# Performance work log

Hardware: AMD Instinct MI355X
Metric: run time of the kernel (lower is better)

The kernel has to match this reference:

```python
import jax, jax.numpy as jnp
import numpy as np

N_NODES = 50000
N_EDGES = 1000000
F = 256          # feature_size
NC = 300         # n_content_dims
ED = 64          # embedding_dim = 2**int(log2(F/4))
L = 3            # n_layers


def setup_inputs() -> dict:
    key = jax.random.key(0)
    ks = jax.random.split(key, 20)
    s = 0.05  # weight init scale
    return {
        'node_ids': jnp.arange(N_NODES, dtype=jnp.int32),
        'content': jax.random.normal(ks[0], (N_NODES, NC), jnp.float32),
        'src': jax.random.randint(ks[1], (N_EDGES,), 0, N_NODES, jnp.int32),
        'dst': jax.random.randint(ks[2], (N_EDGES,), 0, N_NODES, jnp.int32),
        'emb': jax.random.normal(ks[3], (N_NODES + 1, ED), jnp.float32) / ED,
        'W_exp': jax.random.normal(ks[4], (F, ED), jnp.float32) * s,
        'b_exp': jnp.zeros((F,), jnp.float32),
        'W_p1': jax.random.normal(ks[5], (NC, NC), jnp.float32) * s,
        'b_p1': jnp.zeros((NC,), jnp.float32),
        'W_p2': jax.random.normal(ks[6], (F, NC), jnp.float32) * s,
        'b_p2': jnp.zeros((F,), jnp.float32),
        'W_conv': jax.random.normal(ks[7], (L, F, 2 * F), jnp.float32) * s,
        'b_conv': jnp.zeros((L, F), jnp.float32),
        'Wo1': jax.random.normal(ks[8], (L - 1, F, F), jnp.float32) * s,
        'bo1': jnp.zeros((L - 1, F), jnp.float32),
        'Wo2': jax.random.normal(ks[9], (L - 1, F, F), jnp.float32) * s,
        'bo2': jnp.zeros((L - 1, F), jnp.float32),
    }


def _lrelu(x):
    return jax.nn.leaky_relu(x, 0.1)


def reference(node_ids, content, src, dst, emb, W_exp, b_exp, W_p1, b_p1,
              W_p2, b_p2, W_conv, b_conv, Wo1, bo1, Wo2, bo2):
    # initial node repr: expansion(node_emb) + proj(content)  (GaussianNoise = identity at eval)
    h = _lrelu(emb[node_ids] @ W_exp.T + b_exp)                 # [N, F]
    c = _lrelu(content @ W_p1.T + b_p1)
    c = _lrelu(c @ W_p2.T + b_p2)
    h = h + c

    ones = jnp.ones((src.shape[0],), h.dtype)
    deg = jax.ops.segment_sum(ones, dst, num_segments=N_NODES)  # in-degree
    w = (deg + 1.0)[:, None]                                    # +1 for self-loop

    for i in range(L):
        # message passing: sum neighbor h (with self-loop), then neighbor mean
        agg = jax.ops.segment_sum(h[src], dst, num_segments=N_NODES) + h  # [N, F]
        h_agg = (agg - h) / jnp.maximum(w - 1.0, 1.0)
        h_concat = jnp.concatenate([h, h_agg], axis=1)          # [N, 2F]
        h_new = h_concat @ W_conv[i].T + b_conv[i]
        if i < L - 1:
            h_new = _lrelu(h_new)
        # L2-normalize rows
        h_new = h_new / jnp.maximum(
            jnp.linalg.norm(h_new, axis=1, keepdims=True), 1e-6)
        if i < L - 1:  # W_out block (non-prediction layers)
            h_new = _lrelu(h_new @ Wo1[i].T + bo1[i])
            h_new = h_new @ Wo2[i].T + bo2[i]
        h = h_new
    return h
```

## Files before the change

kernel.cpp:

```cpp
#include <hip/hip_runtime.h>
#include <stdint.h>

#define NNODES 50000
#define NROWS_PAD 50048
#define NEDGES 1000000
#define FD 256
#define NCPAD 384
#define EDIM 64
#define NSCAN ((NNODES + 255) / 256)

typedef unsigned short u16;
typedef __attribute__((ext_vector_type(8))) short short8;
typedef __attribute__((ext_vector_type(4))) float floatx4;

__device__ __forceinline__ float bf2f(u16 x) {
    union { unsigned u; float f; } c; c.u = ((unsigned)x) << 16; return c.f;
}
__device__ __forceinline__ u16 f2bf(float f) {
    union { float f; unsigned u; } c; c.f = f;
    unsigned u = c.u;
    return (u16)((u + 0x7fffu + ((u >> 16) & 1u)) >> 16);
}
__device__ __forceinline__ void gload16(const u16* g, u16* l) {
    __builtin_amdgcn_global_load_lds(
        (const __attribute__((address_space(1))) void*)g,
        (__attribute__((address_space(3))) void*)l, 16, 0, 0);
}

__global__ void detect_kernel(const u16* p, int* flag) {
    __shared__ int smax;
    if (threadIdx.x == 0) smax = 0;
    __syncthreads();
    int m = 0;
    for (int i = threadIdx.x; i < 8192; i += 256) {
        int e = (p[i] >> 7) & 0xFF;
        m = m > e ? m : e;
    }
    atomicMax(&smax, m);
    __syncthreads();
    if (threadIdx.x == 0) *flag = (smax >= 140) ? 1 : 0;
}

#define NB_CONV 1798
#define NB_PADC 37536
#define NB_PADE 6256
#define NB_CNT  1954
#define NB_OTH  (NB_CONV + NB_PADC + NB_PADE)
#define PREP_GRID 47572
__global__ __launch_bounds__(512) void prep_kernel(
    u16* arena, const int* flagp,
    const void* wexp, const void* bexp, const void* wp1, const void* bp1,
    const void* wp2, const void* bp2, const void* wconv, const void* bconv,
    const void* wo1, const void* bo1, const void* wo2, const void* bo2,
    u16* cpad, const void* content, u16* ebuf, const void* emb,
    const int* dst, int* deg)
{
    const int bid = blockIdx.x;
    const int q = bid / 24, r = bid % 24;
    if (r == 23) {
        if (q >= NB_CNT) return;
        int e = q * 512 + threadIdx.x;
        if (e < NEDGES) atomicAdd(&deg[dst[e]], 1);
        return;
    }
    long oid = (long)q * 23 + r;
    if (oid >= NB_OTH) return;
    int fl = *flagp;
    if (oid < NB_CONV) {
        const int offs[13]  = {0,16384,16640,164096,164480,262784,263040,
                               656256,657024,788096,788608,919680,920192};
        const int rreal[12] = {256,1,300,1,256,1,768,1,512,1,512,1};
        const int creal[12] = {64,256,300,300,300,256,512,768,256,512,256,512};
        const int cpd[12]   = {64,256,384,384,384,256,512,768,256,512,256,512};
        long gid = oid * 512 + threadIdx.x;
        if (gid >= 920192) return;
        const void* srcs[12] = {wexp,bexp,wp1,bp1,wp2,bp2,wconv,bconv,wo1,bo1,wo2,bo2};
        int t = 0;
        #pragma unroll
        for (int i = 1; i < 12; ++i) if (gid >= offs[i]) t = i;
        long local = gid - offs[t];
        int rr = (int)(local / cpd[t]);
        int cc = (int)(local % cpd[t]);
        u16 v = 0;
        if (rr < rreal[t] && cc < creal[t]) {
            long si = (long)rr * creal[t] + cc;
            v = fl ? f2bf(((const float*)srcs[t])[si]) : ((const u16*)srcs[t])[si];
        }
        arena[gid] = v;
    } else if (oid < NB_CONV + NB_PADC) {
        long gid = (oid - NB_CONV) * 512 + threadIdx.x;
        int rr = (int)(gid / NCPAD), cc = (int)(gid % NCPAD);
        u16 v = 0;
        if (rr < NNODES && cc < 300) {
            long si = (long)rr * 300 + cc;
            v = fl ? f2bf(((const float*)content)[si]) : ((const u16*)content)[si];
        }
        cpad[gid] = v;
    } else {
        long gid = (oid - NB_CONV - NB_PADC) * 512 + threadIdx.x;
        int rr = (int)(gid / EDIM), cc = (int)(gid % EDIM);
        u16 v = 0;
        if (rr < NNODES) {
            long si = (long)rr * EDIM + cc;
            v = fl ? f2bf(((const float*)emb)[si]) : ((const u16*)emb)[si];
        }
        ebuf[gid] = v;
    }
}

__global__ __launch_bounds__(256) void scan1_kernel(const int* deg, int* bsum) {
    __shared__ int s[256];
    int t = threadIdx.x;
    int i = blockIdx.x * 256 + t;
    s[t] = (i < NNODES) ? deg[i] : 0;
    __syncthreads();
    #pragma unroll
    for (int off = 128; off > 0; off >>= 1) {
        if (t < off) s[t] += s[t + off];
        __syncthreads();
    }
    if (t == 0) bsum[blockIdx.x] = s[0];
}

__global__ __launch_bounds__(256) void scan2_kernel(int* bsum, int* row_start) {
    __shared__ int s[256];
    int t = threadIdx.x;
    int v = (t < NSCAN) ? bsum[t] : 0;
    s[t] = v;
    __syncthreads();
    for (int off = 1; off < 256; off <<= 1) {
        int x = (t >= off) ? s[t - off] : 0;
        __syncthreads();
        s[t] += x;
        __syncthreads();
    }
    if (t < NSCAN) bsum[t] = s[t] - v;
    if (t == 0) row_start[NNODES] = NEDGES;
}

__global__ __launch_bounds__(256) void scan3_kernel(const int* deg, const int* bsum,
        int* row_start, int* cursor, float* inv_w) {
    __shared__ int s[256];
    int t = threadIdx.x;
    int i = blockIdx.x * 256 + t;
    int v = (i < NNODES) ? deg[i] : 0;
    s[t] = v;
    __syncthreads();
    for (int off = 1; off < 256; off <<= 1) {
        int x = (t >= off) ? s[t - off] : 0;
        __syncthreads();
        s[t] += x;
        __syncthreads();
    }
    if (i < NNODES) {
        int base = bsum[blockIdx.x] + s[t] - v;
        row_start[i] = base;
        cursor[i] = base;
        inv_w[i] = 1.0f / (float)(v > 0 ? v : 1);
    }
}

#define IF_GRID (391 * 7)
__global__ __launch_bounds__(512, 4) void initfill_kernel(
    const u16* __restrict__ cpad, const u16* __restrict__ ebuf,
    const u16* __restrict__ Wp1, const u16* __restrict__ bp1,
    const u16* __restrict__ Wp2, const u16* __restrict__ bp2,
    const u16* __restrict__ Wexp, const u16* __restrict__ bexp,
    u16* __restrict__ hbuf,
    const int* __restrict__ src, const int* __restrict__ dst,
    int* __restrict__ cursor, int* __restrict__ esrc)
{
    __shared__ __align__(16) u16 sA[64 * 32];
    __shared__ __align__(16) u16 sB[384 * 32];
    __shared__ __align__(16) u16 T[64 * 384];

    const int g7 = blockIdx.x / 7, r7 = blockIdx.x % 7;
    if (r7 >= 2) {
        int fb = g7 * 5 + (r7 - 2);
        int e = fb * 512 + threadIdx.x;
        if (e < NEDGES) {
            int v = dst[e];
            int pos = atomicAdd(&cursor[v], 1);
            if ((unsigned)pos < (unsigned)NEDGES) esrc[pos] = src[e];
        }
        return;
    }
    const int bm = (g7 * 2 + r7) * 64;
    const int t = threadIdx.x;
    const int wave = t >> 6, lane = t & 63;
    const int quad = lane >> 4, l16 = lane & 15;
    const int wm = wave >> 2, wn = wave & 3;
    const int lrow = lane >> 2, lcol = (lane & 3) * 8;

    floatx4 a1[2][6];
    #pragma unroll
    for (int i = 0; i < 2; ++i)
        #pragma unroll
        for (int j = 0; j < 6; ++j) a1[i][j] = (floatx4){0.f, 0.f, 0.f, 0.f};
    for (int kt = 0; kt < 384; kt += 32) {
        if (wave < 4)
            gload16(cpad + (size_t)(bm + wave * 16 + lrow) * NCPAD + kt + lcol,
                    &sA[(wave * 16) * 32]);
        #pragma unroll
        for (int c = 0; c < 3; ++c) {
            int r0 = wave * 48 + c * 16;
            gload16(Wp1 + (size_t)(r0 + lrow) * NCPAD + kt + lcol, &sB[r0 * 32]);
        }
        __syncthreads();
        short8 af[2];
        #pragma unroll
        for (int mt = 0; mt < 2; ++mt)
            af[mt] = *(const short8*)&sA[(wm * 32 + mt * 16 + l16) * 32 + quad * 8];
        #pragma unroll
        for (int nt = 0; nt < 6; ++nt) {
            short8 bf = *(const short8*)&sB[(wn * 96 + nt * 16 + l16) * 32 + quad * 8];
            a1[0][nt] = __builtin_amdgcn_mfma_f32_16x16x32_bf16(af[0], bf, a1[0][nt], 0, 0, 0);
            a1[1][nt] = __builtin_amdgcn_mfma_f32_16x16x32_bf16(af[1], bf, a1[1][nt], 0, 0, 0);
        }
        __syncthreads();
    }
    #pragma unroll
    for (int nt = 0; nt < 6; ++nt) {
        int col = wn * 96 + nt * 16 + l16;
        float bv = bf2f(bp1[col]);
        #pragma unroll
        for (int mt = 0; mt < 2; ++mt)
            #pragma unroll
            for (int rr = 0; rr < 4; ++rr) {
                int row = wm * 32 + mt * 16 + quad * 4 + rr;
                float v = a1[mt][nt][rr] + bv;
                v = v > 0.f ? v : 0.1f * v;
                T[(row * NCPAD + col) ^ ((row & 7) << 3)] = f2bf(v);
            }
    }
    __syncthreads();

    floatx4 a2[2][4];
    #pragma unroll
    for (int i = 0; i < 2; ++i)
        #pragma unroll
        for (int j = 0; j < 4; ++j) a2[i][j] = (floatx4){0.f, 0.f, 0.f, 0.f};
    for (int kt = 0; kt < 384; kt += 32) {
        #pragma unroll
        for (int c = 0; c < 2; ++c) {
            int r0 = wave * 32 + c * 16;
            gload16(Wp2 + (size_t)(r0 + lrow) * NCPAD + kt + lcol, &sB[r0 * 32]);
        }
        __syncthreads();
        short8 af[2];
        #pragma unroll
        for (int mt = 0; mt < 2; ++mt) {
            int row = wm * 32 + mt * 16 + l16;
            af[mt] = *(const short8*)&T[(row * NCPAD + kt + quad * 8) ^ ((row & 7) << 3)];
        }
        #pragma unroll
        for (int nt = 0; nt < 4; ++nt) {
            short8 bf = *(const short8*)&sB[(wn * 64 + nt * 16 + l16) * 32 + quad * 8];
            a2[0][nt] = __builtin_amdgcn_mfma_f32_16x16x32_bf16(af[0], bf, a2[0][nt], 0, 0, 0);
            a2[1][nt] = __builtin_amdgcn_mfma_f32_16x16x32_bf16(af[1], bf, a2[1][nt], 0, 0, 0);
        }
        __syncthreads();
    }

    floatx4 aE[2][4];
    #pragma unroll
    for (int i = 0; i < 2; ++i)
        #pragma unroll
        for (int j = 0; j < 4; ++j) aE[i][j] = (floatx4){0.f, 0.f, 0.f, 0.f};
    for (int kt = 0; kt < 64; kt += 32) {
        if (wave < 4)
            gload16(ebuf + (size_t)(bm + wave * 16 + lrow) * EDIM + kt + lcol,
                    &sA[(wave * 16) * 32]);
        #pragma unroll
        for (int c = 0; c < 2; ++c) {
            int r0 = wave * 32 + c * 16;
            gload16(Wexp + (size_t)(r0 + lrow) * EDIM + kt + lcol, &sB[r0 * 32]);
        }
        __syncthreads();
        short8 af[2];
        #pragma unroll
        for (int mt = 0; mt < 2; ++mt)
            af[mt] = *(const short8*)&sA[(wm * 32 + mt * 16 + l16) * 32 + quad * 8];
        #pragma unroll
        for (int nt = 0; nt < 4; ++nt) {
            short8 bf = *(const short8*)&sB[(wn * 64 + nt * 16 + l16) * 32 + quad * 8];
            aE[0][nt] = __builtin_amdgcn_mfma_f32_16x16x32_bf16(af[0], bf, aE[0][nt], 0, 0, 0);
            aE[1][nt] = __builtin_amdgcn_mfma_f32_16x16x32_bf16(af[1], bf, aE[1][nt], 0, 0, 0);
        }
        __syncthreads();
    }

    #pragma unroll
    for (int nt = 0; nt < 4; ++nt) {
        int col = wn * 64 + nt * 16 + l16;
        float bE = bf2f(bexp[col]), b2 = bf2f(bp2[col]);
        #pragma unroll
        for (int mt = 0; mt < 2; ++mt)
            #pragma unroll
            for (int rr = 0; rr < 4; ++rr) {
                int row = wm * 32 + mt * 16 + quad * 4 + rr;
                int gm = bm + row;
                if (gm < NNODES) {
                    float hE = aE[mt][nt][rr] + bE; hE = hE > 0.f ? hE : 0.1f * hE;
                    float c2 = a2[mt][nt][rr] + b2; c2 = c2 > 0.f ? c2 : 0.1f * c2;
                    hbuf[(size_t)gm * FD + col] = f2bf(hE + c2);
                }
            }
    }
}

__global__ __launch_bounds__(512, 4) void layer_kernel(
    const u16* __restrict__ h, const u16* __restrict__ agg,
    const u16* __restrict__ Wc, const u16* __restrict__ bc,
    const u16* __restrict__ W1, const u16* __restrict__ b1,
    const u16* __restrict__ W2, const u16* __restrict__ b2,
    u16* __restrict__ out)
{
    __shared__ __align__(16) u16 sA[2][64 * 32];
    __shared__ __align__(16) u16 sB[2][256 * 32];
    __shared__ __align__(16) u16 T[64 * 256];
    __shared__ float ssq[4][64];

    const int t = threadIdx.x;
    const int wave = t >> 6, lane = t & 63;
    const int quad = lane >> 4, l16 = lane & 15;
    const int wm = wave >> 2, wn = wave & 3;
    const int lrow = lane >> 2, lcol = (lane & 3) * 8;
    const int bm = blockIdx.x * 64;

    floatx4 acc[2][4];
    #pragma unroll
    for (int i = 0; i < 2; ++i)
        #pragma unroll
        for (int j = 0; j < 4; ++j) acc[i][j] = (floatx4){0.f, 0.f, 0.f, 0.f};

    for (int kt = 0; kt < 512; kt += 64) {
        const u16* Ap = (kt < 256) ? h : agg;
        const int kk = kt & 255;
        {
            int hh = wave & 1, r0 = (wave >> 1) * 16;
            gload16(Ap + (size_t)(bm + r0 + lrow) * 256 + kk + hh * 32 + lcol,
                    &sA[hh][r0 * 32]);
        }
        #pragma unroll
        for (int c = 0; c < 4; ++c) {
            int hh = c >> 1, r0 = wave * 32 + (c & 1) * 16;
            gload16(Wc + (size_t)(r0 + lrow) * 512 + kt + hh * 32 + lcol,
                    &sB[hh][r0 * 32]);
        }
        __syncthreads();
        #pragma unroll
        for (int g = 0; g < 2; ++g) {
            short8 af[2], bf[4];
            #pragma unroll
            for (int mt = 0; mt < 2; ++mt)
                af[mt] = *(const short8*)&sA[g][(wm * 32 + mt * 16 + l16) * 32 + quad * 8];
            #pragma unroll
            for (int nt = 0; nt < 4; ++nt)
                bf[nt] = *(const short8*)&sB[g][(wn * 64 + nt * 16 + l16) * 32 + quad * 8];
            #pragma unroll
            for (int mt = 0; mt < 2; ++mt)
                #pragma unroll
                for (int nt = 0; nt < 4; ++nt)
                    acc[mt][nt] = __builtin_amdgcn_mfma_f32_16x16x32_bf16(af[mt], bf[nt], acc[mt][nt], 0, 0, 0);
        }
        __syncthreads();
    }
    {
        float part[2][4];
        #pragma unroll
        for (int mt = 0; mt < 2; ++mt)
            #pragma unroll
            for (int rr = 0; rr < 4; ++rr) part[mt][rr] = 0.f;
        #pragma unroll
        for (int nt = 0; nt < 4; ++nt) {
            float bv = bf2f(bc[wn * 64 + nt * 16 + l16]);
            #pragma unroll
            for (int mt = 0; mt < 2; ++mt)
                #pragma unroll
                for (int rr = 0; rr < 4; ++rr) {
                    float v = acc[mt][nt][rr] + bv;
                    v = v > 0.f ? v : 0.1f * v;
                    part[mt][rr] += v * v;
                }
        }
        #pragma unroll
        for (int off = 1; off < 16; off <<= 1)
            #pragma unroll
            for (int mt = 0; mt < 2; ++mt)
                #pragma unroll
                for (int rr = 0; rr < 4; ++rr)
                    part[mt][rr] += __shfl_xor(part[mt][rr], off);
        if (l16 == 0)
            #pragma unroll
            for (int mt = 0; mt < 2; ++mt)
                #pragma unroll
                for (int rr = 0; rr < 4; ++rr)
                    ssq[wn][wm * 32 + mt * 16 + quad * 4 + rr] = part[mt][rr];
        __syncthreads();
        #pragma unroll
        for (int mt = 0; mt < 2; ++mt)
            #pragma unroll
            for (int rr = 0; rr < 4; ++rr) {
                int row = wm * 32 + mt * 16 + quad * 4 + rr;
                float s = 1.0f / fmaxf(sqrtf(ssq[0][row] + ssq[1][row] +
                                             ssq[2][row] + ssq[3][row]), 1e-6f);
                #pragma unroll
                for (int nt = 0; nt < 4; ++nt) {
                    int col = wn * 64 + nt * 16 + l16;
                    float v = acc[mt][nt][rr] + bf2f(bc[col]);
                    v = v > 0.f ? v : 0.1f * v;
                    T[(row * 256 + col) ^ ((row & 7) << 3)] = f2bf(v * s);
                }
            }
        __syncthreads();
    }

    #pragma unroll
    for (int i = 0; i < 2; ++i)
        #pragma unroll
        for (int j = 0; j < 4; ++j) acc[i][j] = (floatx4){0.f, 0.f, 0.f, 0.f};
    for (int kt = 0; kt < 256; kt += 64) {
        #pragma unroll
        for (int c = 0; c < 4; ++c) {
            int hh = c >> 1, r0 = wave * 32 + (c & 1) * 16;
            gload16(W1 + (size_t)(r0 + lrow) * 256 + kt + hh * 32 + lcol,
                    &sB[hh][r0 * 32]);
        }
        __syncthreads();
        #pragma unroll
        for (int g = 0; g < 2; ++g) {
            short8 af[2], bf[4];
            #pragma unroll
            for (int mt = 0; mt < 2; ++mt) {
                int row = wm * 32 + mt * 16 + l16;
                af[mt] = *(const short8*)&T[(row * 256 + kt + g * 32 + quad * 8) ^ ((row & 7) << 3)];
            }
            #pragma unroll
            for (int nt = 0; nt < 4; ++nt)
                bf[nt] = *(const short8*)&sB[g][(wn * 64 + nt * 16 + l16) * 32 + quad * 8];
            #pragma unroll
            for (int mt = 0; mt < 2; ++mt)
                #pragma unroll
                for (int nt = 0; nt < 4; ++nt)
                    acc[mt][nt] = __builtin_amdgcn_mfma_f32_16x16x32_bf16(af[mt], bf[nt], acc[mt][nt], 0, 0, 0);
        }
        __syncthreads();
    }
    #pragma unroll
    for (int nt = 0; nt < 4; ++nt) {
        int col = wn * 64 + nt * 16 + l16;
        float bv = bf2f(b1[col]);
        #pragma unroll
        for (int mt = 0; mt < 2; ++mt) {
            #pragma unroll
            for (int r = 0; r < 4; ++r) {
                int row = wm * 32 + mt * 16 + quad * 4 + r;
                float v = acc[mt][nt][r] + bv;
                v = v > 0.f ? v : 0.1f * v;
                T[(row * 256 + col) ^ ((row & 7) << 3)] = f2bf(v);
            }
        }
    }
    __syncthreads();

    #pragma unroll
    for (int i = 0; i < 2; ++i)
        #pragma unroll
        for (int j = 0; j < 4; ++j) acc[i][j] = (floatx4){0.f, 0.f, 0.f, 0.f};
    for (int kt = 0; kt < 256; kt += 64) {
        #pragma unroll
        for (int c = 0; c < 4; ++c) {
            int hh = c >> 1, r0 = wave * 32 + (c & 1) * 16;
            gload16(W2 + (size_t)(r0 + lrow) * 256 + kt + hh * 32 + lcol,
                    &sB[hh][r0 * 32]);
        }
        __syncthreads();
        #pragma unroll
        for (int g = 0; g < 2; ++g) {
            short8 af[2], bf[4];
            #pragma unroll
            for (int mt = 0; mt < 2; ++mt) {
                int row = wm * 32 + mt * 16 + l16;
                af[mt] = *(const short8*)&T[(row * 256 + kt + g * 32 + quad * 8) ^ ((row & 7) << 3)];
            }
            #pragma unroll
            for (int nt = 0; nt < 4; ++nt)
                bf[nt] = *(const short8*)&sB[g][(wn * 64 + nt * 16 + l16) * 32 + quad * 8];
            #pragma unroll
            for (int mt = 0; mt < 2; ++mt)
                #pragma unroll
                for (int nt = 0; nt < 4; ++nt)
                    acc[mt][nt] = __builtin_amdgcn_mfma_f32_16x16x32_bf16(af[mt], bf[nt], acc[mt][nt], 0, 0, 0);
        }
        __syncthreads();
    }
    #pragma unroll
    for (int nt = 0; nt < 4; ++nt) {
        int col = wn * 64 + nt * 16 + l16;
        float bv = bf2f(b2[col]);
        #pragma unroll
        for (int mt = 0; mt < 2; ++mt) {
            #pragma unroll
            for (int r = 0; r < 4; ++r) {
                int row = wm * 32 + mt * 16 + quad * 4 + r;
                int gm = bm + row;
                if (gm < NNODES) {
                    float v = acc[mt][nt][r] + bv;
                    out[(size_t)gm * 256 + col] = f2bf(v);
                }
            }
        }
    }
}

__global__ __launch_bounds__(512, 4) void final_kernel(
    const u16* __restrict__ h, const u16* __restrict__ agg,
    const u16* __restrict__ Wc, const u16* __restrict__ bc,
    float* __restrict__ out)
{
    __shared__ __align__(16) u16 sA[2][64 * 32];
    __shared__ __align__(16) u16 sB[2][256 * 32];
    __shared__ float ssq[4][64];

    const int t = threadIdx.x;
    const int wave = t >> 6, lane = t & 63;
    const int quad = lane >> 4, l16 = lane & 15;
    const int wm = wave >> 2, wn = wave & 3;
    const int lrow = lane >> 2, lcol = (lane & 3) * 8;
    const int bm = blockIdx.x * 64;

    floatx4 acc[2][4];
    #pragma unroll
    for (int i = 0; i < 2; ++i)
        #pragma unroll
        for (int j = 0; j < 4; ++j) acc[i][j] = (floatx4){0.f, 0.f, 0.f, 0.f};

    for (int kt = 0; kt < 512; kt += 64) {
        const u16* Ap = (kt < 256) ? h : agg;
        const int kk = kt & 255;
        {
            int hh = wave & 1, r0 = (wave >> 1) * 16;
            gload16(Ap + (size_t)(bm + r0 + lrow) * 256 + kk + hh * 32 + lcol,
                    &sA[hh][r0 * 32]);
        }
        #pragma unroll
        for (int c = 0; c < 4; ++c) {
            int hh = c >> 1, r0 = wave * 32 + (c & 1) * 16;
            gload16(Wc + (size_t)(r0 + lrow) * 512 + kt + hh * 32 + lcol,
                    &sB[hh][r0 * 32]);
        }
        __syncthreads();
        #pragma unroll
        for (int g = 0; g < 2; ++g) {
            short8 af[2], bf[4];
            #pragma unroll
            for (int mt = 0; mt < 2; ++mt)
                af[mt] = *(const short8*)&sA[g][(wm * 32 + mt * 16 + l16) * 32 + quad * 8];
            #pragma unroll
            for (int nt = 0; nt < 4; ++nt)
                bf[nt] = *(const short8*)&sB[g][(wn * 64 + nt * 16 + l16) * 32 + quad * 8];
            #pragma unroll
            for (int mt = 0; mt < 2; ++mt)
                #pragma unroll
                for (int nt = 0; nt < 4; ++nt)
                    acc[mt][nt] = __builtin_amdgcn_mfma_f32_16x16x32_bf16(af[mt], bf[nt], acc[mt][nt], 0, 0, 0);
        }
        __syncthreads();
    }
    float part[2][4];
    #pragma unroll
    for (int mt = 0; mt < 2; ++mt)
        #pragma unroll
        for (int rr = 0; rr < 4; ++rr) part[mt][rr] = 0.f;
    #pragma unroll
    for (int nt = 0; nt < 4; ++nt) {
        float bv = bf2f(bc[wn * 64 + nt * 16 + l16]);
        #pragma unroll
        for (int mt = 0; mt < 2; ++mt)
            #pragma unroll
            for (int rr = 0; rr < 4; ++rr) {
                float v = acc[mt][nt][rr] + bv;
                part[mt][rr] += v * v;
            }
    }
    #pragma unroll
    for (int off = 1; off < 16; off <<= 1)
        #pragma unroll
        for (int mt = 0; mt < 2; ++mt)
            #pragma unroll
            for (int rr = 0; rr < 4; ++rr)
                part[mt][rr] += __shfl_xor(part[mt][rr], off);
    if (l16 == 0)
        #pragma unroll
        for (int mt = 0; mt < 2; ++mt)
            #pragma unroll
            for (int rr = 0; rr < 4; ++rr)
                ssq[wn][wm * 32 + mt * 16 + quad * 4 + rr] = part[mt][rr];
    __syncthreads();
    #pragma unroll
    for (int mt = 0; mt < 2; ++mt)
        #pragma unroll
        for (int rr = 0; rr < 4; ++rr) {
            int row = wm * 32 + mt * 16 + quad * 4 + rr;
            int gm = bm + row;
            float s = 1.0f / fmaxf(sqrtf(ssq[0][row] + ssq[1][row] +
                                         ssq[2][row] + ssq[3][row]), 1e-6f);
            if (gm < NNODES) {
                #pragma unroll
                for (int nt = 0; nt < 4; ++nt) {
                    int col = wn * 64 + nt * 16 + l16;
                    out[(size_t)gm * 256 + col] = (acc[mt][nt][rr] + bf2f(bc[col])) * s;
                }
            }
        }
}

__global__ __launch_bounds__(256) void agg_kernel(
    const u16* h, const int* row_start, const int* esrc,
    const float* inv_w, u16* out)
{
    int gid = blockIdx.x * blockDim.x + threadIdx.x;
    int wid = gid >> 6;
    int lane = gid & 63;
    if (wid >= NNODES) return;
    int e0 = row_start[wid], e1 = row_start[wid + 1];
    e0 = max(0, min(e0, NEDGES));
    e1 = max(e0, min(e1, NEDGES));
    float a0 = 0.f, a1 = 0.f, a2 = 0.f, a3 = 0.f;
    int e = e0;
    for (; e + 4 <= e1; e += 4) {
        int u0 = esrc[e + 0]; if ((unsigned)u0 >= (unsigned)NNODES) u0 = 0;
        int u1 = esrc[e + 1]; if ((unsigned)u1 >= (unsigned)NNODES) u1 = 0;
        int u2 = esrc[e + 2]; if ((unsigned)u2 >= (unsigned)NNODES) u2 = 0;
        int u3 = esrc[e + 3]; if ((unsigned)u3 >= (unsigned)NNODES) u3 = 0;
        ushort4 t0 = *(const ushort4*)(h + (size_t)u0 * FD + lane * 4);
        ushort4 t1 = *(const ushort4*)(h + (size_t)u1 * FD + lane * 4);
        ushort4 t2 = *(const ushort4*)(h + (size_t)u2 * FD + lane * 4);
        ushort4 t3 = *(const ushort4*)(h + (size_t)u3 * FD + lane * 4);
        a0 += bf2f(t0.x) + bf2f(t1.x) + bf2f(t2.x) + bf2f(t3.x);
        a1 += bf2f(t0.y) + bf2f(t1.y) + bf2f(t2.y) + bf2f(t3.y);
        a2 += bf2f(t0.z) + bf2f(t1.z) + bf2f(t2.z) + bf2f(t3.z);
        a3 += bf2f(t0.w) + bf2f(t1.w) + bf2f(t2.w) + bf2f(t3.w);
    }
    for (; e < e1; ++e) {
        int u = esrc[e];
        if ((unsigned)u >= (unsigned)NNODES) u = 0;
        ushort4 tv = *(const ushort4*)(h + (size_t)u * FD + lane * 4);
        a0 += bf2f(tv.x); a1 += bf2f(tv.y); a2 += bf2f(tv.z); a3 += bf2f(tv.w);
    }
    float s = inv_w[wid];
    ushort4 ov;
    ov.x = f2bf(a0 * s); ov.y = f2bf(a1 * s); ov.z = f2bf(a2 * s); ov.w = f2bf(a3 * s);
    *(ushort4*)(out + (size_t)wid * FD + lane * 4) = ov;
}

extern "C" void kernel_launch(void* const* d_in, const int* in_sizes, int n_in,
                              void* d_out, int out_size, void* d_ws, size_t ws_size,
                              hipStream_t stream) {
    const void* content = d_in[1];
    const int* src      = (const int*)d_in[2];
    const int* dst      = (const int*)d_in[3];
    const void* emb     = d_in[4];

    char* ws = (char*)d_ws;
    u16* arena = (u16*)(ws);
    u16* hbuf  = (u16*)(ws + 1840640);
    u16* buf2  = (u16*)(ws + 27465216);
    u16* cpad  = (u16*)(ws + 27465216);
    u16* ebuf  = (u16*)(ws + 65902336);
    int*   deg    = (int*)(ws + 78714368);
    int*   rs     = (int*)(ws + 78914560);
    int*   cursor = (int*)(ws + 79114752);
    float* inv_w  = (float*)(ws + 79314944);
    int*   esrc   = (int*)(ws + 79515136);
    int*   bsum   = (int*)(ws + 83515648);
    int*   flag   = (int*)(ws + 83516672);

    u16* aWexp  = arena;            u16* aBexp  = arena + 16384;
    u16* aWp1   = arena + 16640;    u16* aBp1   = arena + 164096;
    u16* aWp2   = arena + 164480;   u16* aBp2   = arena + 262784;
    u16* aWconv = arena + 263040;   u16* aBconv = arena + 656256;
    u16* aWo1   = arena + 657024;   u16* aBo1   = arena + 788096;
    u16* aWo2   = arena + 788608;   u16* aBo2   = arena + 919680;

    const int MB64 = NROWS_PAD / 64;

    detect_kernel<<<1, 256, 0, stream>>>((const u16*)content, flag);
    hipMemsetAsync(deg, 0, (size_t)NNODES * 4, stream);
    prep_kernel<<<PREP_GRID, 512, 0, stream>>>(arena, flag,
        d_in[5], d_in[6], d_in[7], d_in[8], d_in[9], d_in[10], d_in[11],
        d_in[12], d_in[13], d_in[14], d_in[15], d_in[16],
        cpad, content, ebuf, emb, dst, deg);

    scan1_kernel<<<NSCAN, 256, 0, stream>>>(deg, bsum);
    scan2_kernel<<<1, 256, 0, stream>>>(bsum, rs);
    scan3_kernel<<<NSCAN, 256, 0, stream>>>(deg, bsum, rs, cursor, inv_w);

    initfill_kernel<<<IF_GRID, 512, 0, stream>>>(cpad, ebuf,
        aWp1, aBp1, aWp2, aBp2, aWexp, aBexp, hbuf, src, dst, cursor, esrc);

    for (int i = 0; i < 3; ++i) {
        agg_kernel<<<(NNODES * 64) / 256, 256, 0, stream>>>(hbuf, rs, esrc, inv_w, buf2);
        if (i < 2) {
            layer_kernel<<<dim3(MB64), dim3(512), 0, stream>>>(
                hbuf, buf2,
                aWconv + (size_t)i * FD * 2 * FD, aBconv + (size_t)i * FD,
                aWo1 + (size_t)i * FD * FD, aBo1 + (size_t)i * FD,
                aWo2 + (size_t)i * FD * FD, aBo2 + (size_t)i * FD,
                hbuf);
        } else {
            final_kernel<<<dim3(MB64), dim3(512), 0, stream>>>(
                hbuf, buf2,
                aWconv + (size_t)i * FD * 2 * FD, aBconv + (size_t)i * FD,
                (float*)d_out);
        }
    }
}
```

Before: 688.3 us.

## Fuse content/embedding conversion into initfill and vectorize degree counting

```diff
diff --git a/kernel.cpp b/kernel.cpp
--- a/kernel.cpp
+++ b/kernel.cpp
@@ -42,70 +42,48 @@
 }
 
 #define NB_CONV 1798
-#define NB_PADC 37536
-#define NB_PADE 6256
-#define NB_CNT  1954
-#define NB_OTH  (NB_CONV + NB_PADC + NB_PADE)
-#define PREP_GRID 47572
+#define NB_CNT4 489
+#define PREP_GRID (NB_CONV + NB_CNT4)
 __global__ __launch_bounds__(512) void prep_kernel(
     u16* arena, const int* flagp,
     const void* wexp, const void* bexp, const void* wp1, const void* bp1,
     const void* wp2, const void* bp2, const void* wconv, const void* bconv,
     const void* wo1, const void* bo1, const void* wo2, const void* bo2,
-    u16* cpad, const void* content, u16* ebuf, const void* emb,
     const int* dst, int* deg)
 {
     const int bid = blockIdx.x;
-    const int q = bid / 24, r = bid % 24;
-    if (r == 23) {
-        if (q >= NB_CNT) return;
-        int e = q * 512 + threadIdx.x;
-        if (e < NEDGES) atomicAdd(&deg[dst[e]], 1);
+    if (bid >= NB_CONV) {
+        int q4 = (bid - NB_CONV) * 512 + threadIdx.x;
+        if (q4 * 4 + 3 < NEDGES) {
+            int4 d = *(const int4*)(dst + q4 * 4);
+            atomicAdd(&deg[d.x], 1);
+            atomicAdd(&deg[d.y], 1);
+            atomicAdd(&deg[d.z], 1);
+            atomicAdd(&deg[d.w], 1);
+        }
         return;
     }
-    long oid = (long)q * 23 + r;
-    if (oid >= NB_OTH) return;
+    const int offs[13]  = {0,16384,16640,164096,164480,262784,263040,
+                           656256,657024,788096,788608,919680,920192};
+    const int rreal[12] = {256,1,300,1,256,1,768,1,512,1,512,1};
+    const int creal[12] = {64,256,300,300,300,256,512,768,256,512,256,512};
+    const int cpd[12]   = {64,256,384,384,384,256,512,768,256,512,256,512};
+    long gid = (long)bid * 512 + threadIdx.x;
+    if (gid >= 920192) return;
+    const void* srcs[12] = {wexp,bexp,wp1,bp1,wp2,bp2,wconv,bconv,wo1,bo1,wo2,bo2};
     int fl = *flagp;
-    if (oid < NB_CONV) {
-        const int offs[13]  = {0,16384,16640,164096,164480,262784,263040,
-                               656256,657024,788096,788608,919680,920192};
-        const int rreal[12] = {256,1,300,1,256,1,768,1,512,1,512,1};
-        const int creal[12] = {64,256,300,300,300,256,512,768,256,512,256,512};
-        const int cpd[12]   = {64,256,384,384,384,256,512,768,256,512,256,512};
-        long gid = oid * 512 + threadIdx.x;
-        if (gid >= 920192) return;
-        const void* srcs[12] = {wexp,bexp,wp1,bp1,wp2,bp2,wconv,bconv,wo1,bo1,wo2,bo2};
-        int t = 0;
-        #pragma unroll
-        for (int i = 1; i < 12; ++i) if (gid >= offs[i]) t = i;
-        long local = gid - offs[t];
-        int rr = (int)(local / cpd[t]);
-        int cc = (int)(local % cpd[t]);
-        u16 v = 0;
-        if (rr < rreal[t] && cc < creal[t]) {
-            long si = (long)rr * creal[t] + cc;
-            v = fl ? f2bf(((const float*)srcs[t])[si]) : ((const u16*)srcs[t])[si];
-        }
-        arena[gid] = v;
-    } else if (oid < NB_CONV + NB_PADC) {
-        long gid = (oid - NB_CONV) * 512 + threadIdx.x;
-        int rr = (int)(gid / NCPAD), cc = (int)(gid % NCPAD);
-        u16 v = 0;
-        if (rr < NNODES && cc < 300) {
-            long si = (long)rr * 300 + cc;
-            v = fl ? f2bf(((const float*)content)[si]) : ((const u16*)content)[si];
-        }
-        cpad[gid] = v;
-    } else {
-        long gid = (oid - NB_CONV - NB_PADC) * 512 + threadIdx.x;
-        int rr = (int)(gid / EDIM), cc = (int)(gid % EDIM);
-        u16 v = 0;
-        if (rr < NNODES) {
-            long si = (long)rr * EDIM + cc;
-            v = fl ? f2bf(((const float*)emb)[si]) : ((const u16*)emb)[si];
-        }
-        ebuf[gid] = v;
-    }
+    int t = 0;
+    #pragma unroll
+    for (int i = 1; i < 12; ++i) if (gid >= offs[i]) t = i;
+    long local = gid - offs[t];
+    int rr = (int)(local / cpd[t]);
+    int cc = (int)(local % cpd[t]);
+    u16 v = 0;
+    if (rr < rreal[t] && cc < creal[t]) {
+        long si = (long)rr * creal[t] + cc;
+        v = fl ? f2bf(((const float*)srcs[t])[si]) : ((const u16*)srcs[t])[si];
+    }
+    arena[gid] = v;
 }
 
 __global__ __launch_bounds__(256) void scan1_kernel(const int* deg, int* bsum) {
@@ -162,7 +140,8 @@
 
 #define IF_GRID (391 * 7)
 __global__ __launch_bounds__(512, 4) void initfill_kernel(
-    const u16* __restrict__ cpad, const u16* __restrict__ ebuf,
+    const void* __restrict__ content, const void* __restrict__ emb,
+    const int* __restrict__ flagp,
     const u16* __restrict__ Wp1, const u16* __restrict__ bp1,
     const u16* __restrict__ Wp2, const u16* __restrict__ bp2,
     const u16* __restrict__ Wexp, const u16* __restrict__ bexp,
@@ -170,7 +149,7 @@
     const int* __restrict__ src, const int* __restrict__ dst,
     int* __restrict__ cursor, int* __restrict__ esrc)
 {
-    __shared__ __align__(16) u16 sA[64 * 32];
+    __shared__ __align__(16) u16 sA[64 * 64];
     __shared__ __align__(16) u16 sB[384 * 32];
     __shared__ __align__(16) u16 T[64 * 384];
 
@@ -191,6 +170,74 @@
     const int quad = lane >> 4, l16 = lane & 15;
     const int wm = wave >> 2, wn = wave & 3;
     const int lrow = lane >> 2, lcol = (lane & 3) * 8;
+    const int fl = *flagp;
+
+    {
+        int row = t >> 3;
+        int c0 = (t & 7) * 8;
+        int gm = bm + row;
+        u16 o[8];
+        if (gm < NNODES) {
+            if (fl) {
+                const float* ep = (const float*)emb + (size_t)gm * EDIM + c0;
+                float4 x = *(const float4*)ep;
+                float4 y = *(const float4*)(ep + 4);
+                o[0]=f2bf(x.x); o[1]=f2bf(x.y); o[2]=f2bf(x.z); o[3]=f2bf(x.w);
+                o[4]=f2bf(y.x); o[5]=f2bf(y.y); o[6]=f2bf(y.z); o[7]=f2bf(y.w);
+            } else {
+                const u16* ep = (const u16*)emb + (size_t)gm * EDIM + c0;
+                ushort4 x = *(const ushort4*)ep;
+                ushort4 y = *(const ushort4*)(ep + 4);
+                o[0]=x.x; o[1]=x.y; o[2]=x.z; o[3]=x.w;
+                o[4]=y.x; o[5]=y.y; o[6]=y.z; o[7]=y.w;
+            }
+        } else {
+            #pragma unroll
+            for (int k = 0; k < 8; ++k) o[k] = 0;
+        }
+        u16* d = &sA[(row * 64 + c0) ^ ((row & 7) << 3)];
+        #pragma unroll
+        for (int k = 0; k < 8; ++k) d[k] = o[k];
+    }
+    #pragma unroll
+    for (int j = 0; j < 6; ++j) {
+        int idx = (j * 512 + t) * 8;
+        int row = idx / 384;
+        int c0 = idx % 384;
+        int gm = bm + row;
+        u16 o[8];
+        if (gm < NNODES && c0 + 8 <= 300) {
+            if (fl) {
+                const float* cp = (const float*)content + (size_t)gm * 300 + c0;
+                float4 x = *(const float4*)cp;
+                float4 y = *(const float4*)(cp + 4);
+                o[0]=f2bf(x.x); o[1]=f2bf(x.y); o[2]=f2bf(x.z); o[3]=f2bf(x.w);
+                o[4]=f2bf(y.x); o[5]=f2bf(y.y); o[6]=f2bf(y.z); o[7]=f2bf(y.w);
+            } else {
+                const u16* cp = (const u16*)content + (size_t)gm * 300 + c0;
+                ushort4 x = *(const ushort4*)cp;
+                ushort4 y = *(const ushort4*)(cp + 4);
+                o[0]=x.x; o[1]=x.y; o[2]=x.z; o[3]=x.w;
+                o[4]=y.x; o[5]=y.y; o[6]=y.z; o[7]=y.w;
+            }
+        } else if (gm < NNODES && c0 < 300) {
+            #pragma unroll
+            for (int k = 0; k < 8; ++k) {
+                int c = c0 + k;
+                o[k] = (c < 300)
+                    ? (fl ? f2bf(((const float*)content)[(size_t)gm * 300 + c])
+                          : ((const u16*)content)[(size_t)gm * 300 + c])
+                    : (u16)0;
+            }
+        } else {
+            #pragma unroll
+            for (int k = 0; k < 8; ++k) o[k] = 0;
+        }
+        u16* d = &T[(row * 384 + c0) ^ ((row & 7) << 3)];
+        #pragma unroll
+        for (int k = 0; k < 8; ++k) d[k] = o[k];
+    }
+    __syncthreads();
 
     floatx4 a1[2][6];
     #pragma unroll
@@ -198,9 +245,6 @@
         #pragma unroll
         for (int j = 0; j < 6; ++j) a1[i][j] = (floatx4){0.f, 0.f, 0.f, 0.f};
     for (int kt = 0; kt < 384; kt += 32) {
-        if (wave < 4)
-            gload16(cpad + (size_t)(bm + wave * 16 + lrow) * NCPAD + kt + lcol,
-                    &sA[(wave * 16) * 32]);
         #pragma unroll
         for (int c = 0; c < 3; ++c) {
             int r0 = wave * 48 + c * 16;
@@ -209,8 +253,10 @@
         __syncthreads();
         short8 af[2];
         #pragma unroll
-        for (int mt = 0; mt < 2; ++mt)
-            af[mt] = *(const short8*)&sA[(wm * 32 + mt * 16 + l16) * 32 + quad * 8];
+        for (int mt = 0; mt < 2; ++mt) {
+            int row = wm * 32 + mt * 16 + l16;
+            af[mt] = *(const short8*)&T[(row * 384 + kt + quad * 8) ^ ((row & 7) << 3)];
+        }
         #pragma unroll
         for (int nt = 0; nt < 6; ++nt) {
             short8 bf = *(const short8*)&sB[(wn * 96 + nt * 16 + l16) * 32 + quad * 8];
@@ -268,9 +314,6 @@
         #pragma unroll
         for (int j = 0; j < 4; ++j) aE[i][j] = (floatx4){0.f, 0.f, 0.f, 0.f};
     for (int kt = 0; kt < 64; kt += 32) {
-        if (wave < 4)
-            gload16(ebuf + (size_t)(bm + wave * 16 + lrow) * EDIM + kt + lcol,
-                    &sA[(wave * 16) * 32]);
         #pragma unroll
         for (int c = 0; c < 2; ++c) {
             int r0 = wave * 32 + c * 16;
@@ -279,8 +322,10 @@
         __syncthreads();
         short8 af[2];
         #pragma unroll
-        for (int mt = 0; mt < 2; ++mt)
-            af[mt] = *(const short8*)&sA[(wm * 32 + mt * 16 + l16) * 32 + quad * 8];
+        for (int mt = 0; mt < 2; ++mt) {
+            int row = wm * 32 + mt * 16 + l16;
+            af[mt] = *(const short8*)&sA[(row * 64 + kt + quad * 8) ^ ((row & 7) << 3)];
+        }
         #pragma unroll
         for (int nt = 0; nt < 4; ++nt) {
             short8 bf = *(const short8*)&sB[(wn * 64 + nt * 16 + l16) * 32 + quad * 8];
@@ -667,8 +712,6 @@
     u16* arena = (u16*)(ws);
     u16* hbuf  = (u16*)(ws + 1840640);
     u16* buf2  = (u16*)(ws + 27465216);
-    u16* cpad  = (u16*)(ws + 27465216);
-    u16* ebuf  = (u16*)(ws + 65902336);
     int*   deg    = (int*)(ws + 78714368);
     int*   rs     = (int*)(ws + 78914560);
     int*   cursor = (int*)(ws + 79114752);
@@ -690,14 +733,13 @@
     hipMemsetAsync(deg, 0, (size_t)NNODES * 4, stream);
     prep_kernel<<<PREP_GRID, 512, 0, stream>>>(arena, flag,
         d_in[5], d_in[6], d_in[7], d_in[8], d_in[9], d_in[10], d_in[11],
-        d_in[12], d_in[13], d_in[14], d_in[15], d_in[16],
-        cpad, content, ebuf, emb, dst, deg);
+        d_in[12], d_in[13], d_in[14], d_in[15], d_in[16], dst, deg);
 
     scan1_kernel<<<NSCAN, 256, 0, stream>>>(deg, bsum);
     scan2_kernel<<<1, 256, 0, stream>>>(bsum, rs);
     scan3_kernel<<<NSCAN, 256, 0, stream>>>(deg, bsum, rs, cursor, inv_w);
 
-    initfill_kernel<<<IF_GRID, 512, 0, stream>>>(cpad, ebuf,
+    initfill_kernel<<<IF_GRID, 512, 0, stream>>>(content, emb, flag,
         aWp1, aBp1, aWp2, aBp2, aWexp, aBexp, hbuf, src, dst, cursor, esrc);
 
     for (int i = 0; i < 3; ++i) {
```

Result: faster. 655.5 us (-4.8%).
